# Performance work log

Measured on AMD Instinct MI355X. Metric: run time of the kernel, lower is better.

Reference implementation:

```python
import jax, jax.numpy as jnp
import numpy as np

B, N = 8, 2048
D_IN, D_FEAT, H, K = 2, 30, 64, 8
D_ATT = D_IN + D_FEAT + H  # 96, per-head attention input dim
ALPHA = 0.2
NEG = -1e9


def setup_inputs() -> dict:
    key = jax.random.key(0)
    ks = jax.random.split(key, 11)
    inputs = jax.random.normal(ks[0], (B, N, D_IN), jnp.float32)
    envs_feat = jax.random.normal(ks[1], (B, N, D_FEAT), jnp.float32)
    state_t = jax.random.normal(ks[2], (B, N, H), jnp.float32)
    conn = jax.random.uniform(ks[3], (N, N)) < 0.05
    conn = conn | jnp.eye(N, dtype=bool)
    bias_mat = jnp.where(conn, 0.0, NEG).astype(jnp.float32)
    # xavier-ish init (gain 1.414)
    def xav(k, shape, fi, fo):
        lim = 1.414 * np.sqrt(6.0 / (fi + fo))
        return jax.random.uniform(k, shape, jnp.float32, -lim, lim)
    W_h = xav(ks[4], (K, D_ATT, H), D_ATT, H)      # stacked per-head W
    a1_h = xav(ks[5], (K, H), H, 1)
    a2_h = xav(ks[6], (K, H), H, 1)
    W_o = xav(ks[7], (K * H, H), K * H, H)
    a1_o = xav(ks[8], (H,), H, 1)
    a2_o = xav(ks[9], (H,), H, 1)
    return {"inputs": inputs, "envs_feat": envs_feat, "state_t": state_t,
            "bias_mat": bias_mat, "W_h": W_h, "a1_h": a1_h, "a2_h": a2_h,
            "W_o": W_o, "a1_o": a1_o, "a2_o": a2_o}


def _gat_multihead(h, bias, W, a1, a2):
    # h: [b,n,d], W: [k,d,h], a1/a2: [k,h], bias: [n,n]
    Wh = jnp.einsum('bnd,kdh->bknh', h, W)
    f1 = jnp.einsum('bknh,kh->bkn', Wh, a1)
    f2 = jnp.einsum('bknh,kh->bkn', Wh, a2)
    e = jax.nn.leaky_relu(f1[:, :, :, None] + f2[:, :, None, :], ALPHA) + bias  # [b,k,n,n]
    att = jax.nn.softmax(e, axis=-1)
    return jnp.einsum('bknm,bkmh->bknh', att, Wh)  # [b,k,n,h]


def _gat_single(h, bias, W, a1, a2):
    # h: [b,n,d], W: [d,h], a1/a2: [h]
    Wh = jnp.einsum('bnd,dh->bnh', h, W)
    f1 = Wh @ a1  # [b,n]
    f2 = Wh @ a2
    e = jax.nn.leaky_relu(f1[:, :, None] + f2[:, None, :], ALPHA) + bias  # [b,n,n]
    att = jax.nn.softmax(e, axis=-1)
    return jnp.einsum('bnm,bmh->bnh', att, Wh)


def reference(inputs, envs_feat, state_t, bias_mat, W_h, a1_h, a2_h, W_o, a1_o, a2_o):
    b, n = inputs.shape[0], inputs.shape[1]
    h = jnp.concatenate([inputs, envs_feat, state_t], axis=2)  # [b,n,D_ATT]
    hp = _gat_multihead(h, bias_mat, W_h, a1_h, a2_h)          # [b,k,n,h]
    h1 = jax.nn.elu(hp)
    h1 = jnp.transpose(h1, (0, 2, 1, 3)).reshape(b, n, -1)     # concat heads: [b,n,k*h]
    out = jax.nn.elu(_gat_single(h1, bias_mat, W_o, a1_o, a2_o))
    return out
```

## Files before the change

### kernel.cpp

```cpp
#include <hip/hip_runtime.h>
#include <hip/hip_bf16.h>
#include <math.h>

#define B   8
#define N   2048
#define DIN 2
#define DF  30
#define HH  64
#define KK  8
#define DATT 96
#define CAP 384
#define CAPL 176
#define ALPHA 0.2f

__device__ __forceinline__ float lrelu(float x) { return x > 0.f ? x : ALPHA * x; }
__device__ __forceinline__ float elu1(float x)  { return x > 0.f ? x : (__expf(x) - 1.f); }
__device__ __forceinline__ unsigned short f2bf(float x) {
    __hip_bfloat16 h = __float2bfloat16(x);
    return *reinterpret_cast<unsigned short*>(&h);
}
__device__ __forceinline__ float bflo(unsigned int u) { return __int_as_float(u << 16); }
__device__ __forceinline__ float bfhi(unsigned int u) { return __int_as_float(u & 0xffff0000u); }

__global__ void k_mask(const float* __restrict__ bias, int* __restrict__ cols,
                       int* __restrict__ cnt) {
    int i = blockIdx.x;
    int lane = threadIdx.x;
    int c = 0;
    for (int j0 = 0; j0 < N; j0 += 64) {
        float v = bias[(size_t)i * N + j0 + lane];
        bool conn = v > -1e8f;
        unsigned long long m = __ballot(conn);
        if (conn) {
            int pos = c + __popcll(m & ((1ull << lane) - 1ull));
            if (pos < CAP) cols[i * CAP + pos] = j0 + lane;
        }
        c += __popcll(m);
    }
    if (lane == 0) cnt[i] = c < CAP ? c : CAP;
}

__global__ void k_wh(const float* __restrict__ inp, const float* __restrict__ envs,
                     const float* __restrict__ st,  const float* __restrict__ W_h,
                     const float* __restrict__ a1,  const float* __restrict__ a2,
                     unsigned short* __restrict__ Whb,
                     float* __restrict__ f1n, float* __restrict__ f2n) {
    __shared__ float Ws[DATT * HH];
    __shared__ float hs[16 * 98];
    int k = blockIdx.y, b = blockIdx.z;
    int i0 = blockIdx.x * 16;
    int tid = threadIdx.x, lane = tid & 63, w = tid >> 6;
    int g = lane >> 4, sub = lane & 15;
    int r = w * 4 + g;

    const float* Wk = W_h + k * DATT * HH;
    for (int idx = tid * 4; idx < DATT * HH; idx += 1024)
        *(float4*)&Ws[idx] = *(const float4*)&Wk[idx];
    {
        int row = tid >> 4, q = tid & 15;
        float4 v = *(const float4*)&st[(size_t)(b * N + i0 + row) * HH + q * 4];
        float* hb = &hs[row * 98 + DIN + DF + q * 4];
        hb[0] = v.x; hb[1] = v.y; hb[2] = v.z; hb[3] = v.w;
    }
    if (tid < 240) {
        int row = tid / 15, q = tid % 15;
        float2 v = *(const float2*)&envs[(size_t)(b * N + i0 + row) * DF + q * 2];
        float* hb = &hs[row * 98 + DIN + q * 2];
        hb[0] = v.x; hb[1] = v.y;
    }
    if (tid < 32) {
        int row = tid >> 1, q = tid & 1;
        hs[row * 98 + q] = inp[(size_t)(b * N + i0 + row) * DIN + q];
    }
    __syncthreads();

    const float* hb = &hs[r * 98];
    float4 acc = make_float4(0.f, 0.f, 0.f, 0.f);
#pragma unroll
    for (int d = 0; d < DATT; d += 2) {
        float2 hv = *(const float2*)&hb[d];
        float4 w0 = *(const float4*)&Ws[d * HH + sub * 4];
        float4 w1 = *(const float4*)&Ws[(d + 1) * HH + sub * 4];
        acc.x += hv.x * w0.x; acc.y += hv.x * w0.y;
        acc.z += hv.x * w0.z; acc.w += hv.x * w0.w;
        acc.x += hv.y * w1.x; acc.y += hv.y * w1.y;
        acc.z += hv.y * w1.z; acc.w += hv.y * w1.w;
    }
    int i = i0 + r;
    unsigned int lo = (unsigned)f2bf(acc.x) | ((unsigned)f2bf(acc.y) << 16);
    unsigned int hi = (unsigned)f2bf(acc.z) | ((unsigned)f2bf(acc.w) << 16);
    *(uint2*)&Whb[((size_t)(b * N + i)) * (KK * HH) + k * HH + sub * 4] = make_uint2(lo, hi);
    float4 a1v = *(const float4*)&a1[k * HH + sub * 4];
    float4 a2v = *(const float4*)&a2[k * HH + sub * 4];
    float p1 = acc.x * a1v.x + acc.y * a1v.y + acc.z * a1v.z + acc.w * a1v.w;
    float p2 = acc.x * a2v.x + acc.y * a2v.y + acc.z * a2v.z + acc.w * a2v.w;
#pragma unroll
    for (int off = 8; off; off >>= 1) {
        p1 += __shfl_xor(p1, off);
        p2 += __shfl_xor(p2, off);
    }
    if (sub == 0) {
        f1n[((size_t)(b * N + i)) * KK + k] = p1;
        f2n[((size_t)(b * N + i)) * KK + k] = p2;
    }
}

__global__ void k_attn(const unsigned short* __restrict__ Whb, const float* __restrict__ f1n,
                       const float* __restrict__ f2n, const int* __restrict__ cols,
                       const int* __restrict__ cnt, float* __restrict__ h1) {
    __shared__ float sw[4][CAPL + 8][8];
    __shared__ int   jl[4][CAPL];
    int flat = blockIdx.y * (N / 4) + blockIdx.x;
    int b = flat & 7, tile = flat >> 3;
    int tid = threadIdx.x, lane = tid & 63, w = tid >> 6;
    int i = tile * 4 + w;
    int k = lane >> 3, q = lane & 7;

    int c = cnt[i]; if (c > CAPL) c = CAPL;
    const int* cl = cols + (size_t)i * CAP;
    for (int e = lane; e < c; e += 64) jl[w][e] = cl[e];

    float f1k = f1n[((size_t)(b * N + i)) * KK + k];
    const float* f2b = f2n + (size_t)b * N * KK;

    float mk = -1e30f;
    for (int e0 = 0; e0 < c; e0 += 8) {
        int e = e0 + q;
        int ee = e < c ? e : c - 1;
        int j = jl[w][ee];
        float s = lrelu(f1k + f2b[(size_t)j * KK + k]);
        if (e >= c) s = -1e30f;
        sw[w][e][k] = s;
        mk = fmaxf(mk, s);
    }
#pragma unroll
    for (int off = 4; off; off >>= 1) mk = fmaxf(mk, __shfl_xor(mk, off));

    float Zk = 0.f;
    for (int e0 = 0; e0 < c; e0 += 8) {
        int e = e0 + q;
        float wt = __expf(sw[w][e][k] - mk);
        sw[w][e][k] = wt;
        Zk += wt;
    }
#pragma unroll
    for (int off = 4; off; off >>= 1) Zk += __shfl_xor(Zk, off);
    float invZ = 1.f / Zk;

    const char* Wp = (const char*)Whb + (size_t)b * N * 1024;
    float4 aL = make_float4(0.f, 0.f, 0.f, 0.f);
    float4 aH = make_float4(0.f, 0.f, 0.f, 0.f);
    int lane16 = lane << 4;
#pragma unroll 8
    for (int e = 0; e < c; ++e) {
        int j = __builtin_amdgcn_readfirstlane(jl[w][e]);
        float wt = sw[w][e][k];
        uint4 v = *(const uint4*)(Wp + ((size_t)j << 10) + lane16);
        aL.x += wt * bflo(v.x); aL.y += wt * bfhi(v.x);
        aL.z += wt * bflo(v.y); aL.w += wt * bfhi(v.y);
        aH.x += wt * bflo(v.z); aH.y += wt * bfhi(v.z);
        aH.z += wt * bflo(v.w); aH.w += wt * bfhi(v.w);
    }
    float4 o1, o2;
    o1.x = elu1(aL.x * invZ); o1.y = elu1(aL.y * invZ);
    o1.z = elu1(aL.z * invZ); o1.w = elu1(aL.w * invZ);
    o2.x = elu1(aH.x * invZ); o2.y = elu1(aH.y * invZ);
    o2.z = elu1(aH.z * invZ); o2.w = elu1(aH.w * invZ);
    float* hp = &h1[((size_t)(b * N + i)) * (KK * HH) + lane * 8];
    *(float4*)hp = o1;
    *(float4*)(hp + 4) = o2;
}

__global__ void k_who(const float* __restrict__ h1, const float* __restrict__ W_o,
                      const float* __restrict__ a1o, const float* __restrict__ a2o,
                      float* __restrict__ Who, float* __restrict__ f1o,
                      float* __restrict__ f2o) {
    __shared__ float Ws[128 * HH];
    int tid = threadIdx.x, lane = tid & 63, w = tid >> 6;
    int g = lane >> 4, sub = lane & 15;
    int row = blockIdx.x * 16 + w * 4 + g;
    const float* hp = h1 + (size_t)row * (KK * HH);
    float4 acc = make_float4(0.f, 0.f, 0.f, 0.f);
    for (int ph = 0; ph < 4; ++ph) {
        __syncthreads();
        for (int idx = tid * 4; idx < 128 * HH; idx += 1024)
            *(float4*)&Ws[idx] = *(const float4*)&W_o[ph * 128 * HH + idx];
        __syncthreads();
#pragma unroll 4
        for (int d0 = 0; d0 < 128; d0 += 4) {
            float4 hv = *(const float4*)(hp + ph * 128 + d0);
#pragma unroll
            for (int dd = 0; dd < 4; ++dd) {
                float hsv = dd == 0 ? hv.x : dd == 1 ? hv.y : dd == 2 ? hv.z : hv.w;
                float4 wv = *(const float4*)&Ws[(d0 + dd) * HH + sub * 4];
                acc.x += hsv * wv.x; acc.y += hsv * wv.y;
                acc.z += hsv * wv.z; acc.w += hsv * wv.w;
            }
        }
    }
    *(float4*)&Who[(size_t)row * HH + sub * 4] = acc;
    float4 a1v = *(const float4*)&a1o[sub * 4];
    float4 a2v = *(const float4*)&a2o[sub * 4];
    float p1 = acc.x * a1v.x + acc.y * a1v.y + acc.z * a1v.z + acc.w * a1v.w;
    float p2 = acc.x * a2v.x + acc.y * a2v.y + acc.z * a2v.z + acc.w * a2v.w;
#pragma unroll
    for (int off = 8; off; off >>= 1) {
        p1 += __shfl_xor(p1, off);
        p2 += __shfl_xor(p2, off);
    }
    if (sub == 0) { f1o[row] = p1; f2o[row] = p2; }
}

__global__ void k_attn2(const float* __restrict__ Who, const float* __restrict__ f1o,
                        const float* __restrict__ f2o, const int* __restrict__ cols,
                        const int* __restrict__ cnt, float* __restrict__ out) {
    __shared__ float sw[4][CAPL + 64];
    __shared__ int   jl[4][CAPL];
    int flat = blockIdx.y * (N / 4) + blockIdx.x;
    int b = flat & 7, tile = flat >> 3;
    int tid = threadIdx.x, lane = tid & 63, w = tid >> 6;
    int i = tile * 4 + w;

    int c = cnt[i]; if (c > CAPL) c = CAPL;
    const int* cl = cols + (size_t)i * CAP;
    for (int e = lane; e < c; e += 64) jl[w][e] = cl[e];

    float f1i = f1o[b * N + i];
    const float* f2p = f2o + (size_t)b * N;

    float m = -1e30f;
    for (int e0 = 0; e0 < c; e0 += 64) {
        int e = e0 + lane;
        int ee = e < c ? e : c - 1;
        int j = jl[w][ee];
        float s = lrelu(f1i + f2p[j]);
        if (e >= c) s = -1e30f;
        sw[w][e] = s;
        m = fmaxf(m, s);
    }
#pragma unroll
    for (int off = 32; off; off >>= 1) m = fmaxf(m, __shfl_xor(m, off));

    float Z = 0.f;
    for (int e0 = 0; e0 < c; e0 += 64) {
        int e = e0 + lane;
        float wt = __expf(sw[w][e] - m);
        sw[w][e] = wt;
        Z += wt;
    }
#pragma unroll
    for (int off = 32; off; off >>= 1) Z += __shfl_xor(Z, off);
    float invZ = 1.f / Z;

    const float* Wp = Who + (size_t)b * N * HH;
    float acc = 0.f;
#pragma unroll 8
    for (int e = 0; e < c; ++e) {
        int j = __builtin_amdgcn_readfirstlane(jl[w][e]);
        float wt = sw[w][e];
        acc += wt * Wp[((size_t)j << 6) + lane];
    }
    out[((size_t)(b * N + i)) * HH + lane] = elu1(acc * invZ);
}

extern "C" void kernel_launch(void* const* d_in, const int* in_sizes, int n_in,
                              void* d_out, int out_size, void* d_ws, size_t ws_size,
                              hipStream_t stream) {
    const float* inp   = (const float*)d_in[0];
    const float* envs  = (const float*)d_in[1];
    const float* st    = (const float*)d_in[2];
    const float* bias  = (const float*)d_in[3];
    const float* W_h   = (const float*)d_in[4];
    const float* a1_h  = (const float*)d_in[5];
    const float* a2_h  = (const float*)d_in[6];
    const float* W_o   = (const float*)d_in[7];
    const float* a1_o  = (const float*)d_in[8];
    const float* a2_o  = (const float*)d_in[9];
    float* out = (float*)d_out;

    char* ws = (char*)d_ws;
    size_t off = 0;
    unsigned short* Whb = (unsigned short*)(ws + off); off += (size_t)B * N * KK * HH * 2;
    float* f1n = (float*)(ws + off); off += (size_t)B * N * KK * 4;
    float* f2n = (float*)(ws + off); off += (size_t)B * N * KK * 4;
    float* h1  = (float*)(ws + off); off += (size_t)B * N * KK * HH * 4;
    float* Who = (float*)(ws + off); off += (size_t)B * N * HH * 4;
    float* f1o = (float*)(ws + off); off += (size_t)B * N * 4;
    float* f2o = (float*)(ws + off); off += (size_t)B * N * 4;
    int*   cols = (int*)(ws + off);  off += (size_t)N * CAP * 4;
    int*   cnt  = (int*)(ws + off);  off += (size_t)N * 4;

    k_mask<<<dim3(N), dim3(64), 0, stream>>>(bias, cols, cnt);
    k_wh<<<dim3(N / 16, KK, B), dim3(256), 0, stream>>>(inp, envs, st, W_h, a1_h, a2_h,
                                                        Whb, f1n, f2n);
    k_attn<<<dim3(N / 4, B), dim3(256), 0, stream>>>(Whb, f1n, f2n, cols, cnt, h1);
    k_who<<<dim3(B * N / 16), dim3(256), 0, stream>>>(h1, W_o, a1_o, a2_o, Who, f1o, f2o);
    k_attn2<<<dim3(N / 4, B), dim3(256), 0, stream>>>(Who, f1o, f2o, cols, cnt, out);
}
```

Before: 319.5 us.

## Repack attn2 to 16 rows per block with float4 gathers; bf16 attention weights

k_attn2 now gives each block 16 rows, with 16 lanes per row. Each lane gathers float4 slices of Who, using packed (byte-offset, weight) pairs held in shared memory. This cuts the number of blocks and widens each load. k_attn keeps its scores in registers through a fixed 22-step unrolled loop and stores the softmax weights as bf16 in LDS, halving LDS traffic at some precision cost. The unrolled loop also reads and writes swb entries beyond c, up to 176. It relies on padded -1e30 scores becoming zero weights and on CAPL+8 rows of headroom.

```diff
diff --git a/kernel.cpp b/kernel.cpp
--- a/kernel.cpp
+++ b/kernel.cpp
@@ -108,8 +108,8 @@
 __global__ void k_attn(const unsigned short* __restrict__ Whb, const float* __restrict__ f1n,
                        const float* __restrict__ f2n, const int* __restrict__ cols,
                        const int* __restrict__ cnt, float* __restrict__ h1) {
-    __shared__ float sw[4][CAPL + 8][8];
-    __shared__ int   jl[4][CAPL];
+    __shared__ unsigned short swb[4][CAPL + 8][8];
+    __shared__ int jl[4][CAPL];
     int flat = blockIdx.y * (N / 4) + blockIdx.x;
     int b = flat & 7, tile = flat >> 3;
     int tid = threadIdx.x, lane = tid & 63, w = tid >> 6;
@@ -123,25 +123,27 @@
     float f1k = f1n[((size_t)(b * N + i)) * KK + k];
     const float* f2b = f2n + (size_t)b * N * KK;
 
+    float s[22];
     float mk = -1e30f;
-    for (int e0 = 0; e0 < c; e0 += 8) {
-        int e = e0 + q;
+#pragma unroll
+    for (int t = 0; t < 22; ++t) {
+        int e = t * 8 + q;
         int ee = e < c ? e : c - 1;
         int j = jl[w][ee];
-        float s = lrelu(f1k + f2b[(size_t)j * KK + k]);
-        if (e >= c) s = -1e30f;
-        sw[w][e][k] = s;
-        mk = fmaxf(mk, s);
+        float sc = lrelu(f1k + f2b[j * KK + k]);
+        if (e >= c) sc = -1e30f;
+        s[t] = sc;
+        mk = fmaxf(mk, sc);
     }
 #pragma unroll
     for (int off = 4; off; off >>= 1) mk = fmaxf(mk, __shfl_xor(mk, off));
 
     float Zk = 0.f;
-    for (int e0 = 0; e0 < c; e0 += 8) {
-        int e = e0 + q;
-        float wt = __expf(sw[w][e][k] - mk);
-        sw[w][e][k] = wt;
+#pragma unroll
+    for (int t = 0; t < 22; ++t) {
+        float wt = __expf(s[t] - mk);
         Zk += wt;
+        swb[w][t * 8 + q][k] = f2bf(wt);
     }
 #pragma unroll
     for (int off = 4; off; off >>= 1) Zk += __shfl_xor(Zk, off);
@@ -154,7 +156,7 @@
 #pragma unroll 8
     for (int e = 0; e < c; ++e) {
         int j = __builtin_amdgcn_readfirstlane(jl[w][e]);
-        float wt = sw[w][e][k];
+        float wt = __int_as_float((unsigned)swb[w][e][k] << 16);
         uint4 v = *(const uint4*)(Wp + ((size_t)j << 10) + lane16);
         aL.x += wt * bflo(v.x); aL.y += wt * bfhi(v.x);
         aL.z += wt * bflo(v.y); aL.w += wt * bfhi(v.y);
@@ -214,53 +216,73 @@
 __global__ void k_attn2(const float* __restrict__ Who, const float* __restrict__ f1o,
                         const float* __restrict__ f2o, const int* __restrict__ cols,
                         const int* __restrict__ cnt, float* __restrict__ out) {
-    __shared__ float sw[4][CAPL + 64];
-    __shared__ int   jl[4][CAPL];
-    int flat = blockIdx.y * (N / 4) + blockIdx.x;
-    int b = flat & 7, tile = flat >> 3;
-    int tid = threadIdx.x, lane = tid & 63, w = tid >> 6;
-    int i = tile * 4 + w;
+    __shared__ float2 sedge[16][CAPL + 2];
+    int flat = blockIdx.y * 128 + blockIdx.x;
+    int b = flat & 7;
+    int tile = flat >> 3;
+    int tid = threadIdx.x;
+    int lane = tid & 63, w = tid >> 6;
+    int g = lane >> 4, sub = lane & 15;
+    int r = w * 4 + g;
+    int i = tile * 16 + r;
 
     int c = cnt[i]; if (c > CAPL) c = CAPL;
+    float f1i = f1o[b * N + i];
     const int* cl = cols + (size_t)i * CAP;
-    for (int e = lane; e < c; e += 64) jl[w][e] = cl[e];
-
-    float f1i = f1o[b * N + i];
     const float* f2p = f2o + (size_t)b * N;
 
     float m = -1e30f;
-    for (int e0 = 0; e0 < c; e0 += 64) {
-        int e = e0 + lane;
-        int ee = e < c ? e : c - 1;
-        int j = jl[w][ee];
-        float s = lrelu(f1i + f2p[j]);
-        if (e >= c) s = -1e30f;
-        sw[w][e] = s;
-        m = fmaxf(m, s);
-    }
-#pragma unroll
-    for (int off = 32; off; off >>= 1) m = fmaxf(m, __shfl_xor(m, off));
+    for (int e = sub; e < c; e += 16) {
+        int j = cl[e];
+        float sc = lrelu(f1i + f2p[j]);
+        sedge[r][e] = make_float2(__int_as_float(j << 8), sc);
+        m = fmaxf(m, sc);
+    }
+#pragma unroll
+    for (int off = 8; off; off >>= 1) m = fmaxf(m, __shfl_xor(m, off));
 
     float Z = 0.f;
-    for (int e0 = 0; e0 < c; e0 += 64) {
-        int e = e0 + lane;
-        float wt = __expf(sw[w][e] - m);
-        sw[w][e] = wt;
+    for (int e = sub; e < c; e += 16) {
+        float wt = __expf(sedge[r][e].y - m);
+        sedge[r][e].y = wt;
         Z += wt;
     }
 #pragma unroll
-    for (int off = 32; off; off >>= 1) Z += __shfl_xor(Z, off);
+    for (int off = 8; off; off >>= 1) Z += __shfl_xor(Z, off);
     float invZ = 1.f / Z;
 
-    const float* Wp = Who + (size_t)b * N * HH;
-    float acc = 0.f;
-#pragma unroll 8
-    for (int e = 0; e < c; ++e) {
-        int j = __builtin_amdgcn_readfirstlane(jl[w][e]);
-        float wt = sw[w][e];
-        acc += wt * Wp[((size_t)j << 6) + lane];
-    }
-    out[((size_t)(b * N + i)) * HH + lane] = elu1(acc * invZ);
+    const char* Wp = (const char*)(Who + (size_t)b * N * HH);
+    int lane4 = sub << 4;
+    float4 acc = make_float4(0.f, 0.f, 0.f, 0.f);
+    int e = 0;
+    for (; e + 4 <= c; e += 4) {
+        float2 p0 = sedge[r][e];
+        float2 p1 = sedge[r][e + 1];
+        float2 p2 = sedge[r][e + 2];
+        float2 p3 = sedge[r][e + 3];
+        float4 v0 = *(const float4*)(Wp + (__float_as_int(p0.x) + lane4));
+        float4 v1 = *(const float4*)(Wp + (__float_as_int(p1.x) + lane4));
+        float4 v2 = *(const float4*)(Wp + (__float_as_int(p2.x) + lane4));
+        float4 v3 = *(const float4*)(Wp + (__float_as_int(p3.x) + lane4));
+        acc.x += p0.y * v0.x; acc.y += p0.y * v0.y;
+        acc.z += p0.y * v0.z; acc.w += p0.y * v0.w;
+        acc.x += p1.y * v1.x; acc.y += p1.y * v1.y;
+        acc.z += p1.y * v1.z; acc.w += p1.y * v1.w;
+        acc.x += p2.y * v2.x; acc.y += p2.y * v2.y;
+        acc.z += p2.y * v2.z; acc.w += p2.y * v2.w;
+        acc.x += p3.y * v3.x; acc.y += p3.y * v3.y;
+        acc.z += p3.y * v3.z; acc.w += p3.y * v3.w;
+    }
+    for (; e < c; ++e) {
+        float2 p0 = sedge[r][e];
+        float4 v0 = *(const float4*)(Wp + (__float_as_int(p0.x) + lane4));
+        acc.x += p0.y * v0.x; acc.y += p0.y * v0.y;
+        acc.z += p0.y * v0.z; acc.w += p0.y * v0.w;
+    }
+    float4 o;
+    o.x = elu1(acc.x * invZ); o.y = elu1(acc.y * invZ);
+    o.z = elu1(acc.z * invZ); o.w = elu1(acc.w * invZ);
+    *(float4*)&out[(size_t)(b * N + i) * HH + sub * 4] = o;
 }
 
 extern "C" void kernel_launch(void* const* d_in, const int* in_sizes, int n_in,
@@ -295,5 +317,5 @@
                                                         Whb, f1n, f2n);
     k_attn<<<dim3(N / 4, B), dim3(256), 0, stream>>>(Whb, f1n, f2n, cols, cnt, h1);
     k_who<<<dim3(B * N / 16), dim3(256), 0, stream>>>(h1, W_o, a1_o, a2_o, Who, f1o, f2o);
-    k_attn2<<<dim3(N / 4, B), dim3(256), 0, stream>>>(Who, f1o, f2o, cols, cnt, out);
-}
+    k_attn2<<<dim3(N / 16, B), dim3(256), 0, stream>>>(Who, f1o, f2o, cols, cnt, out);
+}
```

After: 275.1 us. -13.9%, faster.
